# Kernel optimization log

Measured on AMD Instinct MI355X. Metric: run time of the kernel, lower is better.

The kernel has to match this reference:

```python
import jax, jax.numpy as jnp
import numpy as np

ROUTINGS = 3
EPS = 1e-7  # tf.keras.backend.epsilon()


def _squash(s):
    # s: (B, num_caps, cap_dim)
    n = jnp.linalg.norm(s, axis=-1, keepdims=True)
    return (n ** 2 / (1.0 + n ** 2)) * s / (n + EPS)


def setup_inputs() -> dict:
    key = jax.random.key(0)
    k1, k2 = jax.random.split(key)
    B, N, D_IN, M, C = 64, 2048, 16, 32, 16
    inputs = jax.random.normal(k1, (B, N, D_IN), dtype=jnp.float32)
    # he_normal: std = sqrt(2 / fan_in), fan_in = D_IN for the (1, D_IN, M*C) kernel
    W = jax.random.normal(k2, (D_IN, M, C), dtype=jnp.float32) * np.float32(np.sqrt(2.0 / D_IN))
    return {"inputs": inputs, "W": W}


def reference(inputs, W):
    # prediction vectors u_hat: (B, N, num_caps, cap_dim)
    u_hat = jnp.einsum('bnd,dmc->bnmc', inputs, W)
    b = jnp.zeros(u_hat.shape[:3], dtype=u_hat.dtype)  # (B, N, num_caps)
    v = None
    for _ in range(ROUTINGS):  # fixed small routing count
        c = jax.nn.softmax(b, axis=1)                      # over input capsules
        s = jnp.einsum('bnm,bnmc->bmc', c, u_hat)          # weighted sum
        v = _squash(s)                                     # (B, num_caps, cap_dim)
        b = b + jnp.einsum('bmc,bnmc->bnm', v, u_hat)      # agreement update
    return v
```

## Files before the change

kernel.cpp:

```cpp
#include <hip/hip_runtime.h>
#include <math.h>


#define TPB 512

#define DPP_ADDF(x, ctrl) \
    ((x) + __int_as_float(__builtin_amdgcn_update_dpp( \
        0, __float_as_int(x), (ctrl), 0xF, 0xF, true)))

__global__ __launch_bounds__(TPB, 4)
void capsule_routing_kernel(const float* __restrict__ in,
                            const float* __restrict__ W,
                            float* __restrict__ out)
{
    __shared__ float red[8 * 34];
    __shared__ float fin[34];
    __shared__ float cum[32];
    __shared__ float w_lds[16 * 33];

    const int tid = threadIdx.x;
    const int w   = tid >> 6;
    const int l   = tid & 63;
    const int c4  = l & 3;
    const int b   = blockIdx.x & 63;
    const int m0  = (blockIdx.x >> 6) << 1;

    const float4* __restrict__ inb4 =
        (const float4*)(in + ((size_t)b << 15)) + ((w << 10) + l);

    {
        const int d = tid >> 5, r = tid & 31;
        w_lds[d * 33 + r] = W[(d << 9) + (m0 << 4) + r];
    }
    __syncthreads();

    for (int pass = 0; pass < 3; ++pass) {
        float wv0[4], wv1[4];
        if (pass) {
            #pragma unroll
            for (int j = 0; j < 4; ++j) {
                wv0[j] = cum[(c4 << 2) + j];
                wv1[j] = cum[16 + (c4 << 2) + j];
            }
        }

        float S0 = 0.f, S1 = 0.f;
        float x0[4] = {0.f, 0.f, 0.f, 0.f};
        float x1[4] = {0.f, 0.f, 0.f, 0.f};

        #pragma unroll 4
        for (int g = 0; g < 16; ++g) {
            const float4 f = inb4[g << 6];
            if (pass) {
                float d0 = f.x*wv0[0] + f.y*wv0[1] + f.z*wv0[2] + f.w*wv0[3];
                float d1 = f.x*wv1[0] + f.y*wv1[1] + f.z*wv1[2] + f.w*wv1[3];
                d0 = DPP_ADDF(d0, 0xB1); d0 = DPP_ADDF(d0, 0x4E);
                d1 = DPP_ADDF(d1, 0xB1); d1 = DPP_ADDF(d1, 0x4E);
                const float e0 = __expf(d0);
                const float e1 = __expf(d1);
                S0 += e0; S1 += e1;
                x0[0] += e0*f.x; x0[1] += e0*f.y; x0[2] += e0*f.z; x0[3] += e0*f.w;
                x1[0] += e1*f.x; x1[1] += e1*f.y; x1[2] += e1*f.z; x1[3] += e1*f.w;
            } else {
                x0[0] += f.x; x0[1] += f.y; x0[2] += f.z; x0[3] += f.w;
            }
        }
        if (!pass) {
            #pragma unroll
            for (int j = 0; j < 4; ++j) x1[j] = x0[j];
        }

        float vals[10] = { x0[0], x0[1], x0[2], x0[3],
                           x1[0], x1[1], x1[2], x1[3], S0, S1 };
        #pragma unroll
        for (int v = 0; v < 10; ++v) {
            float x = vals[v];
            x = DPP_ADDF(x, 0x104);
            x = DPP_ADDF(x, 0x108);
            x += __shfl_xor(x, 16);
            x += __shfl_xor(x, 32);
            vals[v] = x;
        }
        if (l < 4) {
            float* rp = &red[w * 34];
            #pragma unroll
            for (int j = 0; j < 4; ++j) {
                rp[1 + (c4 << 2) + j]      = vals[j];
                rp[18 + (c4 << 2) + j]     = vals[4 + j];
            }
            if (l == 0) {
                rp[0]  = pass ? vals[8] : 256.f;
                rp[17] = pass ? vals[9] : 256.f;
            }
        }
        __syncthreads();
        if (tid < 34) {
            float a = 0.f;
            #pragma unroll
            for (int w2 = 0; w2 < 8; ++w2) a += red[w2 * 34 + tid];
            fin[tid] = a;
        }
        __syncthreads();

        if (tid < 32) {
            const int tmi = tid >> 4;
            const int tc  = tid & 15;
            const float rS = 1.f / fin[tmi * 17];
            float s = 0.f;
            #pragma unroll
            for (int d = 0; d < 16; ++d)
                s += fin[tmi * 17 + 1 + d] * w_lds[d * 33 + (tmi << 4) + tc];
            s *= rS;
            float n2 = s * s;
            n2 += __shfl_xor(n2, 1);
            n2 += __shfl_xor(n2, 2);
            n2 += __shfl_xor(n2, 4);
            n2 += __shfl_xor(n2, 8);
            const float nr = sqrtf(n2);
            const float v  = s * (n2 / (1.f + n2)) / (nr + 1e-7f);
            if (pass < 2) {
                float wvv = 0.f;
                #pragma unroll
                for (int c2 = 0; c2 < 16; ++c2)
                    wvv += w_lds[tc * 33 + (tmi << 4) + c2] * __shfl(v, (tmi << 4) + c2);
                if (pass == 0) cum[(tmi << 4) + tc] = wvv;
                else           cum[(tmi << 4) + tc] += wvv;
            } else {
                out[((size_t)b << 9) + ((m0 + tmi) << 4) + tc] = v;
            }
        }
        __syncthreads();
    }
}

extern "C" void kernel_launch(void* const* d_in, const int* in_sizes, int n_in,
                              void* d_out, int out_size, void* d_ws, size_t ws_size,
                              hipStream_t stream) {
    (void)in_sizes; (void)n_in; (void)d_ws; (void)ws_size; (void)out_size;
    const float* in = (const float*)d_in[0];
    const float* W  = (const float*)d_in[1];
    float* out = (float*)d_out;
    hipLaunchKernelGGL(capsule_routing_kernel, dim3(1024), dim3(TPB), 0, stream,
                       in, W, out);
}
```

Before: 83.21 us.

## Stage batch input in LDS as bf16 and route 16 capsules per block with MFMA

Each block now covers one batch and 16 output capsules, for 128 blocks instead of 1024. It loads the batch's input once into LDS as bf16, in both row-major and transposed copies. The agreement logits and the exp-weighted sums are computed with bf16 16x16x32 MFMA instructions instead of scalar FMAs, and the routing vector is stored as a bf16 value pre-scaled by log2e so exp2 can be used. This removes the repeated global re-reads of the input across capsule-pair blocks and moves the dot products onto matrix cores. In exchange it uses a very large LDS footprint, gives fewer blocks and lower occupancy, and loses precision from bf16 rounding of the inputs, exponentials and logits.

```diff
diff --git a/kernel.cpp b/kernel.cpp
--- a/kernel.cpp
+++ b/kernel.cpp
@@ -3,114 +3,146 @@
 
 
 #define TPB 512
+#define LOG2E 1.44269504088896f
+
+typedef __attribute__((ext_vector_type(8))) short short8;
+typedef __attribute__((ext_vector_type(4))) float float4v;
 
 #define DPP_ADDF(x, ctrl) \
     ((x) + __int_as_float(__builtin_amdgcn_update_dpp( \
         0, __float_as_int(x), (ctrl), 0xF, 0xF, true)))
 
-__global__ __launch_bounds__(TPB, 4)
+static __device__ inline unsigned short f2bf(float x) {
+    unsigned u = __float_as_uint(x);
+    return (unsigned short)((u + 0x7FFFu + ((u >> 16) & 1u)) >> 16);
+}
+static __device__ inline unsigned pk2(float a, float b) {
+    return (unsigned)f2bf(a) | ((unsigned)f2bf(b) << 16);
+}
+
+__global__ __launch_bounds__(TPB, 2)
 void capsule_routing_kernel(const float* __restrict__ in,
                             const float* __restrict__ W,
                             float* __restrict__ out)
 {
-    __shared__ float red[8 * 34];
-    __shared__ float fin[34];
-    __shared__ float cum[32];
-    __shared__ float w_lds[16 * 33];
+    __shared__ unsigned short innorm[2048 * 16];
+    __shared__ unsigned short inT[16 * 2056];
+    __shared__ unsigned short e_all[8][16 * 36];
+    __shared__ float red[8 * 288];
+    __shared__ float sum0[32 * 20];
+    __shared__ unsigned short cum_lds[16 * 16];
 
-    const int tid = threadIdx.x;
-    const int w   = tid >> 6;
-    const int l   = tid & 63;
-    const int c4  = l & 3;
-    const int b   = blockIdx.x & 63;
-    const int m0  = (blockIdx.x >> 6) << 1;
-
-    const float4* __restrict__ inb4 =
-        (const float4*)(in + ((size_t)b << 15)) + ((w << 10) + l);
+    const int tid  = threadIdx.x;
+    const int w    = tid >> 6;
+    const int l    = tid & 63;
+    const int ml   = l & 15;
+    const int quad = l >> 4;
+    const int b    = blockIdx.x & 63;
+    const int m0g  = (blockIdx.x >> 6) << 4;
 
     {
-        const int d = tid >> 5, r = tid & 31;
-        w_lds[d * 33 + r] = W[(d << 9) + (m0 << 4) + r];
+        const float4* gin = (const float4*)(in + ((size_t)b << 15));
+        float c0 = 0.f, c1 = 0.f, c2 = 0.f, c3 = 0.f;
+        const int d0 = (tid & 3) * 4;
+        #pragma unroll
+        for (int k = 0; k < 16; ++k) {
+            const int idx = tid + TPB * k;
+            const float4 g = gin[idx];
+            const int n = idx >> 2;
+            c0 += g.x; c1 += g.y; c2 += g.z; c3 += g.w;
+            const unsigned short u0 = f2bf(g.x), u1 = f2bf(g.y),
+                                 u2 = f2bf(g.z), u3 = f2bf(g.w);
+            uint2 pk; pk.x = (unsigned)u0 | ((unsigned)u1 << 16);
+                      pk.y = (unsigned)u2 | ((unsigned)u3 << 16);
+            *(uint2*)&innorm[n * 16 + d0] = pk;
+            inT[(d0 + 0) * 2056 + n] = u0;
+            inT[(d0 + 1) * 2056 + n] = u1;
+            inT[(d0 + 2) * 2056 + n] = u2;
+            inT[(d0 + 3) * 2056 + n] = u3;
+        }
+        c0 = DPP_ADDF(c0, 0x104); c0 = DPP_ADDF(c0, 0x108);
+        c1 = DPP_ADDF(c1, 0x104); c1 = DPP_ADDF(c1, 0x108);
+        c2 = DPP_ADDF(c2, 0x104); c2 = DPP_ADDF(c2, 0x108);
+        c3 = DPP_ADDF(c3, 0x104); c3 = DPP_ADDF(c3, 0x108);
+        if ((l & 15) < 4) {
+            float4 v4; v4.x = c0; v4.y = c1; v4.z = c2; v4.w = c3;
+            *(float4*)&sum0[((w << 2) + quad) * 20 + (l & 3) * 4] = v4;
+        }
     }
     __syncthreads();
 
+    float cwv = 0.f;
+
     for (int pass = 0; pass < 3; ++pass) {
-        float wv0[4], wv1[4];
         if (pass) {
+            short8 bc = {0,0,0,0,0,0,0,0};
+            if (quad < 2) {
+                #pragma unroll
+                for (int j = 0; j < 8; ++j)
+                    bc[j] = (short)cum_lds[(quad * 8 + j) * 16 + ml];
+            }
+            float4v xc = {0.f, 0.f, 0.f, 0.f};
+            float Sp = 0.f;
+            unsigned short* ew = &e_all[w][0];
+
+            #pragma unroll 2
+            for (int t = 0; t < 8; ++t) {
+                const int nb = (w << 8) + (t << 5);
+                short8 a0 = {0,0,0,0,0,0,0,0};
+                short8 a1 = {0,0,0,0,0,0,0,0};
+                if (quad < 2) {
+                    a0 = *(const short8*)&innorm[(nb + ml) * 16 + quad * 8];
+                    a1 = *(const short8*)&innorm[(nb + 16 + ml) * 16 + quad * 8];
+                }
+                const float4v z = {0.f, 0.f, 0.f, 0.f};
+                float4v c0 = __builtin_amdgcn_mfma_f32_16x16x32_bf16(a0, bc, z, 0, 0, 0);
+                float4v c1 = __builtin_amdgcn_mfma_f32_16x16x32_bf16(a1, bc, z, 0, 0, 0);
+                float e00 = exp2f(c0[0]), e01 = exp2f(c0[1]),
+                      e02 = exp2f(c0[2]), e03 = exp2f(c0[3]);
+                float e10 = exp2f(c1[0]), e11 = exp2f(c1[1]),
+                      e12 = exp2f(c1[2]), e13 = exp2f(c1[3]);
+                Sp += (e00 + e01) + (e02 + e03) + (e10 + e11) + (e12 + e13);
+                uint2 w0; w0.x = pk2(e00, e01); w0.y = pk2(e02, e03);
+                uint2 w1; w1.x = pk2(e10, e11); w1.y = pk2(e12, e13);
+                *(uint2*)&ew[ml * 36 + quad * 4]      = w0;
+                *(uint2*)&ew[ml * 36 + 16 + quad * 4] = w1;
+                union { uint2 u2v[2]; short8 s; } ua;
+                ua.u2v[0] = *(const uint2*)&ew[ml * 36 + quad * 8];
+                ua.u2v[1] = *(const uint2*)&ew[ml * 36 + quad * 8 + 4];
+                const short8 bi = *(const short8*)&inT[ml * 2056 + nb + quad * 8];
+                xc = __builtin_amdgcn_mfma_f32_16x16x32_bf16(ua.s, bi, xc, 0, 0, 0);
+            }
+            Sp += __shfl_xor(Sp, 16);
+            Sp += __shfl_xor(Sp, 32);
+            if (l < 16) red[w * 288 + 272 + l] = Sp;
             #pragma unroll
-            for (int j = 0; j < 4; ++j) {
-                wv0[j] = cum[(c4 << 2) + j];
-                wv1[j] = cum[16 + (c4 << 2) + j];
-            }
-        }
-
-        float S0 = 0.f, S1 = 0.f;
-        float x0[4] = {0.f, 0.f, 0.f, 0.f};
-        float x1[4] = {0.f, 0.f, 0.f, 0.f};
-
-        #pragma unroll 4
-        for (int g = 0; g < 16; ++g) {
-            const float4 f = inb4[g << 6];
-            if (pass) {
-                float d0 = f.x*wv0[0] + f.y*wv0[1] + f.z*wv0[2] + f.w*wv0[3];
-                float d1 = f.x*wv1[0] + f.y*wv1[1] + f.z*wv1[2] + f.w*wv1[3];
-                d0 = DPP_ADDF(d0, 0xB1); d0 = DPP_ADDF(d0, 0x4E);
-                d1 = DPP_ADDF(d1, 0xB1); d1 = DPP_ADDF(d1, 0x4E);
-                const float e0 = __expf(d0);
-                const float e1 = __expf(d1);
-                S0 += e0; S1 += e1;
-                x0[0] += e0*f.x; x0[1] += e0*f.y; x0[2] += e0*f.z; x0[3] += e0*f.w;
-                x1[0] += e1*f.x; x1[1] += e1*f.y; x1[2] += e1*f.z; x1[3] += e1*f.w;
-            } else {
-                x0[0] += f.x; x0[1] += f.y; x0[2] += f.z; x0[3] += f.w;
-            }
-        }
-        if (!pass) {
-            #pragma unroll
-            for (int j = 0; j < 4; ++j) x1[j] = x0[j];
-        }
-
-        float vals[10] = { x0[0], x0[1], x0[2], x0[3],
-                           x1[0], x1[1], x1[2], x1[3], S0, S1 };
-        #pragma unroll
-        for (int v = 0; v < 10; ++v) {
-            float x = vals[v];
-            x = DPP_ADDF(x, 0x104);
-            x = DPP_ADDF(x, 0x108);
-            x += __shfl_xor(x, 16);
-            x += __shfl_xor(x, 32);
-            vals[v] = x;
-        }
-        if (l < 4) {
-            float* rp = &red[w * 34];
-            #pragma unroll
-            for (int j = 0; j < 4; ++j) {
-                rp[1 + (c4 << 2) + j]      = vals[j];
-                rp[18 + (c4 << 2) + j]     = vals[4 + j];
-            }
-            if (l == 0) {
-                rp[0]  = pass ? vals[8] : 256.f;
-                rp[17] = pass ? vals[9] : 256.f;
-            }
-        }
-        __syncthreads();
-        if (tid < 34) {
-            float a = 0.f;
-            #pragma unroll
-            for (int w2 = 0; w2 < 8; ++w2) a += red[w2 * 34 + tid];
-            fin[tid] = a;
+            for (int r = 0; r < 4; ++r)
+                red[w * 288 + (quad * 4 + r) * 17 + ml] = xc[r];
         }
         __syncthreads();
 
-        if (tid < 32) {
-            const int tmi = tid >> 4;
-            const int tc  = tid & 15;
-            const float rS = 1.f / fin[tmi * 17];
+        if (tid < 256) {
+            const int m  = tid >> 4;
+            const int tc = tid & 15;
+            const int lbase = tid & 48;
+            float Stot, xtot = 0.f;
+            if (pass == 0) {
+                Stot = 2048.f;
+                #pragma unroll 8
+                for (int q = 0; q < 32; ++q) xtot += sum0[q * 20 + tc];
+            } else {
+                Stot = 0.f;
+                #pragma unroll
+                for (int w2 = 0; w2 < 8; ++w2) {
+                    Stot += red[w2 * 288 + 272 + m];
+                    xtot += red[w2 * 288 + m * 17 + tc];
+                }
+            }
             float s = 0.f;
             #pragma unroll
             for (int d = 0; d < 16; ++d)
-                s += fin[tmi * 17 + 1 + d] * w_lds[d * 33 + (tmi << 4) + tc];
-            s *= rS;
+                s += __shfl(xtot, lbase + d) * W[(d << 9) + ((m0g + m) << 4) + tc];
+            s /= Stot;
             float n2 = s * s;
             n2 += __shfl_xor(n2, 1);
             n2 += __shfl_xor(n2, 2);
@@ -122,14 +154,14 @@
                 float wvv = 0.f;
                 #pragma unroll
                 for (int c2 = 0; c2 < 16; ++c2)
-                    wvv += w_lds[tc * 33 + (tmi << 4) + c2] * __shfl(v, (tmi << 4) + c2);
-                if (pass == 0) cum[(tmi << 4) + tc] = wvv;
-                else           cum[(tmi << 4) + tc] += wvv;
+                    wvv += W[(tc << 9) + ((m0g + m) << 4) + c2] * __shfl(v, lbase + c2);
+                cwv += wvv;
+                cum_lds[tc * 16 + m] = f2bf(cwv * LOG2E);
             } else {
-                out[((size_t)b << 9) + ((m0 + tmi) << 4) + tc] = v;
+                out[((size_t)b << 9) + ((m0g + m) << 4) + tc] = v;
             }
         }
-        __syncthreads();
+        if (pass < 2) __syncthreads();
     }
 }
 
@@ -140,6 +172,6 @@
     const float* in = (const float*)d_in[0];
     const float* W  = (const float*)d_in[1];
     float* out = (float*)d_out;
-    hipLaunchKernelGGL(capsule_routing_kernel, dim3(1024), dim3(TPB), 0, stream,
+    hipLaunchKernelGGL(capsule_routing_kernel, dim3(128), dim3(TPB), 0, stream,
                        in, W, out);
 }
```

Result: faster. 71.25 us (-14.4%).
